# Kernel optimization log

Hardware: AMD Instinct MI355X
Metric: run time of the kernel (lower is better)

The kernel has to match this reference:

```python
import jax, jax.numpy as jnp
import numpy as np

BATCH, SEQ_LEN, D_MODEL = 8, 2048, 1024


def setup_inputs() -> dict:
    key = jax.random.key(0)
    ks = jax.random.split(key, 12)
    s = 0.02  # small init scale (stand-in for xavier)
    D, L = D_MODEL, SEQ_LEN
    return {
        "x": jax.random.normal(ks[0], (BATCH, L, D), jnp.float32),
        "W_B": jax.random.normal(ks[1], (D, D), jnp.float32) * s,
        "b_B": jnp.zeros((D,), jnp.float32),
        "W_C": jax.random.normal(ks[2], (D, D), jnp.float32) * s,
        "b_C": jnp.zeros((D,), jnp.float32),
        "W_d": jax.random.normal(ks[3], (D, D), jnp.float32) * s,
        "b_d": jnp.zeros((D,), jnp.float32),
        "delta_p": jax.random.normal(ks[4], (1, L, D), jnp.float32) * s,  # self.delta
        "A": jax.random.normal(ks[5], (L, D), jnp.float32) * s,
        "W_st": jax.random.normal(ks[6], (D, D), jnp.float32) * s,  # SToken fc1 Linear
        "b_st": jnp.zeros((D,), jnp.float32),
        "st_bias": jax.random.normal(ks[7], (1, 1, D), jnp.float32) * s,  # SToken bias
    }


def reference(x, W_B, b_B, W_C, b_C, W_d, b_d, delta_p, A, W_st, b_st, st_bias):
    # x: [B, L, D]
    z = jax.nn.sigmoid(x)
    B0 = x @ W_B.T + b_B          # LN_B(x)
    C = x @ W_C.T + b_C           # LN_C(x)

    # SToken: squeeze over seq, Linear -> ReLU -> Sigmoid, + bias, * x
    sq = jnp.mean(x, axis=1, keepdims=True)                    # [B, 1, D]
    sq = jax.nn.sigmoid(jax.nn.relu(sq @ W_st.T + b_st))
    T = (sq + st_bias) * x                                     # [B, L, D]

    delta = jax.nn.sigmoid(x @ W_d.T + b_d + delta_p)          # [B, L, D]
    A_ = delta * A                                             # broadcast [L, D]
    B_ = delta * B0

    # diagonal state-space recurrence: s_t = A_t * s_{t-1} + B_t * x_t; y_t = C_t * s_t + T_t
    def step(s, inputs):
        a_t, b_t, c_t, x_t, t_t = inputs                       # each [B, D]
        s = a_t * s + b_t * x_t
        y = c_t * s + t_t
        return s, y

    s0 = jnp.zeros((x.shape[0], x.shape[2]), x.dtype)
    xs = tuple(jnp.swapaxes(a, 0, 1) for a in (A_, B_, C, x, T))  # [L, B, D]
    _, ys = jax.lax.scan(step, s0, xs)
    x_out = jnp.swapaxes(ys, 0, 1) * z                         # [B, L, D]
    return x_out
```

## Files before the change

kernel.cpp:

```cpp
#include <hip/hip_runtime.h>
#include <hip/hip_bf16.h>
#include <cstdint>
#include <cstddef>

#define D_MODEL 1024
#define SEQ     2048
#define BATCH   8
#define M_TOT   (BATCH*SEQ)
#define N_TOT   (3*D_MODEL)
#define K_TOT   D_MODEL
#define KTILES  (K_TOT/64)
#define NCH     64
#define LCH     (SEQ/NCH)
#define W_UP    8

typedef unsigned short u16;
typedef __attribute__((ext_vector_type(8))) short short8;
typedef __attribute__((ext_vector_type(4))) float f32x4;

__device__ __forceinline__ u16 f2bf(float f) {
    __hip_bfloat16 h = __float2bfloat16(f);
    return __builtin_bit_cast(u16, h);
}
__device__ __forceinline__ uint packbf(float lo, float hi) {
    return (uint)f2bf(lo) | ((uint)f2bf(hi) << 16);
}
__device__ __forceinline__ float bf2f(u16 u) {
    __hip_bfloat16 h = __builtin_bit_cast(__hip_bfloat16, u);
    return __bfloat162float(h);
}
__device__ __forceinline__ float sigmoidf(float v) {
    return 1.0f / (1.0f + __expf(-v));
}
__device__ __forceinline__ void gld_lds16(const void* g, void* l) {
    __builtin_amdgcn_global_load_lds((const __attribute__((address_space(1))) void*)g,
                                     (__attribute__((address_space(3))) void*)l, 16, 0, 0);
}
__device__ __forceinline__ void wg_barrier() {
    asm volatile("" ::: "memory");
    __builtin_amdgcn_s_barrier();
    asm volatile("" ::: "memory");
}

__global__ void k_convert(const float* __restrict__ x, u16* __restrict__ xb,
                          float* __restrict__ sq,
                          const float* __restrict__ WB, const float* __restrict__ WC,
                          const float* __restrict__ Wd, u16* __restrict__ wcat,
                          const float* __restrict__ dp, const float* __restrict__ Aar,
                          uint2* __restrict__ dpA) {
    int bid = blockIdx.x;
    if (bid < 512) {
        int tblk = bid & 63, b = bid >> 6;
        int d = threadIdx.x * 4;
        size_t base = ((size_t)b * SEQ + (size_t)tblk * 32) * D_MODEL + d;
        float s0 = 0.f, s1 = 0.f, s2 = 0.f, s3 = 0.f;
        for (int t = 0; t < 32; ++t) {
            float4 v = *(const float4*)&x[base + (size_t)t * D_MODEL];
            s0 += v.x; s1 += v.y; s2 += v.z; s3 += v.w;
            ushort4 o = make_ushort4(f2bf(v.x), f2bf(v.y), f2bf(v.z), f2bf(v.w));
            *(ushort4*)&xb[base + (size_t)t * D_MODEL] = o;
        }
        atomicAdd(&sq[b * D_MODEL + d + 0], s0);
        atomicAdd(&sq[b * D_MODEL + d + 1], s1);
        atomicAdd(&sq[b * D_MODEL + d + 2], s2);
        atomicAdd(&sq[b * D_MODEL + d + 3], s3);
    } else if (bid < 3584) {
        int tg = (bid - 512) * 256 + threadIdx.x;
        size_t e0 = (size_t)tg * 4;
        int n = (int)(e0 >> 10), k0 = (int)(e0 & 1023);
        const float* W = (n < 1024) ? (WB + (size_t)n * 1024)
                       : (n < 2048) ? (WC + (size_t)(n - 1024) * 1024)
                                    : (Wd + (size_t)(n - 2048) * 1024);
        float4 v = *(const float4*)&W[k0];
        wcat[e0 + 0] = f2bf(v.x);
        wcat[e0 + 1] = f2bf(v.y);
        wcat[e0 + 2] = f2bf(v.z);
        wcat[e0 + 3] = f2bf(v.w);
    } else {
        int tg = (bid - 3584) * 256 + threadIdx.x;
        size_t e0 = (size_t)tg * 8;
        float4 d0 = *(const float4*)&dp[e0];
        float4 d1 = *(const float4*)&dp[e0 + 4];
        float4 a0 = *(const float4*)&Aar[e0];
        float4 a1 = *(const float4*)&Aar[e0 + 4];
        uint2* o = &dpA[e0 >> 1];
        o[0] = make_uint2(packbf(d0.x, d0.y), packbf(a0.x, a0.y));
        o[1] = make_uint2(packbf(d0.z, d0.w), packbf(a0.z, a0.w));
        o[2] = make_uint2(packbf(d1.x, d1.y), packbf(a1.x, a1.y));
        o[3] = make_uint2(packbf(d1.z, d1.w), packbf(a1.z, a1.w));
    }
}

__global__ void k_stoken(const float* __restrict__ sq, const float* __restrict__ Wst,
                         float* __restrict__ stacc) {
    __shared__ float s[BATCH][64];
    int nb = blockIdx.x & 3, ks = blockIdx.x >> 2;
    int k0 = ks * 64;
    for (int i = threadIdx.x; i < BATCH * 64; i += 256)
        s[i >> 6][i & 63] = sq[(i >> 6) * D_MODEL + k0 + (i & 63)] * (1.0f / SEQ);
    __syncthreads();
    int n = nb * 256 + threadIdx.x;
    const float* w = Wst + (size_t)n * D_MODEL + k0;
    float acc[BATCH] = {};
    for (int k = 0; k < 64; k += 4) {
        float4 wv = *(const float4*)&w[k];
#pragma unroll
        for (int b = 0; b < BATCH; ++b)
            acc[b] += s[b][k] * wv.x + s[b][k+1] * wv.y + s[b][k+2] * wv.z + s[b][k+3] * wv.w;
    }
#pragma unroll
    for (int b = 0; b < BATCH; ++b)
        atomicAdd(&stacc[b * D_MODEL + n], acc[b]);
}

__device__ __forceinline__ u16* slab_ptr(u16* ls, int buf, int ab, int kk) {
    return ls + (size_t)((((buf << 1) | ab) << 1) | kk) * 8192;
}

__device__ __forceinline__ short8 ldsfrag(const u16* slab, int R, int g) {
    int off = R * 64 + ((g ^ ((R >> 1) & 3)) << 4);
    return *(const short8*)((const char*)slab + off);
}

__device__ __forceinline__ void stage2(const u16* __restrict__ A, const u16* __restrict__ Bm,
                                       u16* ls, int buf, int kk, int ktile,
                                       int i0, int n0, int w, int l) {
    int srow = l >> 2;
    int scol = ((l & 3) ^ ((l >> 3) & 3)) << 4;
    int kbyte = (ktile * 64 + kk * 32) * 2;
    u16* la = slab_ptr(ls, buf, 0, kk);
    u16* lb = slab_ptr(ls, buf, 1, kk);
#pragma unroll
    for (int j = 0; j < 2; ++j) {
        int s = 2 * w + j;
        int row = s * 16 + srow;
        gld_lds16((const char*)(A  + (size_t)(i0 + row) * K_TOT) + kbyte + scol,
                  (char*)la + s * 1024);
        gld_lds16((const char*)(Bm + (size_t)(n0 + row) * K_TOT) + kbyte + scol,
                  (char*)lb + s * 1024);
    }
}

template<bool SG>
__device__ __forceinline__ void kgroup(const u16* __restrict__ A, const u16* __restrict__ Bm,
                                       u16* ls, int t, int i0, int n0,
                                       int wM, int wN, int w, int l, int r, int g,
                                       f32x4 acc[8][4]) {
    const int buf = t & 1;
    const int RA = wM * 128 + r;
    const int RB = wN * 64 + r;

    asm volatile("s_waitcnt vmcnt(0)" ::: "memory");
    wg_barrier();
    if (SG) {
        stage2(A, Bm, ls, buf ^ 1, 0, t + 1, i0, n0, w, l);
        stage2(A, Bm, ls, buf ^ 1, 1, t + 1, i0, n0, w, l);
    }

    const u16* As0 = slab_ptr(ls, buf, 0, 0);
    const u16* Bs0 = slab_ptr(ls, buf, 1, 0);
    const u16* As1 = slab_ptr(ls, buf, 0, 1);
    const u16* Bs1 = slab_ptr(ls, buf, 1, 1);
    short8 a0[4], a1[4], b0[4], b1[4];

#pragma unroll
    for (int m = 0; m < 4; ++m) a0[m] = ldsfrag(As0, RA + m * 16, g);
#pragma unroll
    for (int n = 0; n < 4; ++n) b0[n] = ldsfrag(Bs0, RB + n * 16, g);
#pragma unroll
    for (int m = 0; m < 4; ++m) a1[m] = ldsfrag(As1, RA + m * 16, g);
#pragma unroll
    for (int n = 0; n < 4; ++n) b1[n] = ldsfrag(Bs1, RB + n * 16, g);

    __builtin_amdgcn_s_setprio(1);
#pragma unroll
    for (int m = 0; m < 4; ++m)
#pragma unroll
        for (int n = 0; n < 4; ++n)
            acc[m][n] = __builtin_amdgcn_mfma_f32_16x16x32_bf16(a0[m], b0[n], acc[m][n], 0, 0, 0);
    __builtin_amdgcn_s_setprio(0);

#pragma unroll
    for (int m = 0; m < 4; ++m) a0[m] = ldsfrag(As0, RA + 64 + m * 16, g);

    __builtin_amdgcn_s_setprio(1);
#pragma unroll
    for (int m = 0; m < 4; ++m)
#pragma unroll
        for (int n = 0; n < 4; ++n)
            acc[m][n] = __builtin_amdgcn_mfma_f32_16x16x32_bf16(a1[m], b1[n], acc[m][n], 0, 0, 0);
    __builtin_amdgcn_s_setprio(0);

#pragma unroll
    for (int m = 0; m < 4; ++m) a1[m] = ldsfrag(As1, RA + 64 + m * 16, g);

    __builtin_amdgcn_s_setprio(1);
#pragma unroll
    for (int m = 0; m < 4; ++m)
#pragma unroll
        for (int n = 0; n < 4; ++n)
            acc[4 + m][n] = __builtin_amdgcn_mfma_f32_16x16x32_bf16(a0[m], b0[n], acc[4 + m][n], 0, 0, 0);
#pragma unroll
    for (int m = 0; m < 4; ++m)
#pragma unroll
        for (int n = 0; n < 4; ++n)
            acc[4 + m][n] = __builtin_amdgcn_mfma_f32_16x16x32_bf16(a1[m], b1[n], acc[4 + m][n], 0, 0, 0);
    __builtin_amdgcn_s_setprio(0);
}

__global__ __launch_bounds__(512, 2) void k_gemm(const u16* __restrict__ A,
                                                 const u16* __restrict__ Bm,
                                                 u16* __restrict__ Cout) {
    __shared__ u16 ls[8 * 8192];
    const int tid = threadIdx.x;
    const int l = tid & 63, w = tid >> 6;
    const int wM = w >> 2, wN = w & 3;
    const int r = l & 15, g = l >> 4;
    const int i0 = blockIdx.y * 256;
    const int n0 = blockIdx.x * 256;

    f32x4 acc[8][4] = {};

    stage2(A, Bm, ls, 0, 0, 0, i0, n0, w, l);
    stage2(A, Bm, ls, 0, 1, 0, i0, n0, w, l);

    for (int t = 0; t < KTILES - 1; ++t)
        kgroup<true>(A, Bm, ls, t, i0, n0, wM, wN, w, l, r, g, acc);
    kgroup<false>(A, Bm, ls, KTILES - 1, i0, n0, wM, wN, w, l, r, g, acc);

#pragma unroll
    for (int mi = 0; mi < 8; ++mi)
#pragma unroll
        for (int n = 0; n < 4; ++n)
#pragma unroll
            for (int j = 0; j < 4; ++j) {
                size_t row = (size_t)(i0 + wM * 128 + mi * 16 + g * 4 + j);
                size_t col = (size_t)(n0 + wN * 64 + n * 16 + r);
                Cout[row * N_TOT + col] = f2bf(acc[mi][n][j]);
            }
}

__global__ void k_scan(const u16* __restrict__ xb, const u16* __restrict__ g3,
                       const uint2* __restrict__ dpA,
                       const float* __restrict__ bB, const float* __restrict__ bC,
                       const float* __restrict__ bd, const float* __restrict__ stacc,
                       const float* __restrict__ bst, const float* __restrict__ stb,
                       float* __restrict__ out) {
    int bid = blockIdx.x;
    int dblk = bid & 1, c = (bid >> 1) & (NCH - 1), b = bid >> 7;
    int d = dblk * 512 + threadIdx.x * 2;

    float2 bBv = *(const float2*)&bB[d];
    float2 bdv = *(const float2*)&bd[d];
    float2 bCv = *(const float2*)&bC[d];
    float2 sav = *(const float2*)&stacc[b * D_MODEL + d];
    float2 bstv = *(const float2*)&bst[d];
    float2 stbv = *(const float2*)&stb[d];
    float tc0 = sigmoidf(fmaxf(sav.x + bstv.x, 0.f)) + stbv.x;
    float tc1 = sigmoidf(fmaxf(sav.y + bstv.y, 0.f)) + stbv.y;

    int t0 = c * LCH;
    int tw = (c == 0) ? 0 : t0 - W_UP;
    float s0 = 0.f, s1 = 0.f;

    size_t xoff = ((size_t)b * SEQ + tw) * D_MODEL + d;
    size_t goff = ((size_t)b * SEQ + tw) * N_TOT + d;
    size_t ipa  = ((size_t)tw * D_MODEL + d) >> 1;

    for (int t = tw; t < t0; ++t) {
        uint xu = *(const uint*)&xb[xoff];
        uint gB = *(const uint*)&g3[goff];
        uint gd = *(const uint*)&g3[goff + 2048];
        uint2 pa = dpA[ipa];
        float x0 = bf2f((u16)(xu & 0xffff)), x1 = bf2f((u16)(xu >> 16));
        float b00 = bf2f((u16)(gB & 0xffff)) + bBv.x;
        float b01 = bf2f((u16)(gB >> 16)) + bBv.y;
        float de0 = sigmoidf(bf2f((u16)(gd & 0xffff)) + bdv.x + bf2f((u16)(pa.x & 0xffff)));
        float de1 = sigmoidf(bf2f((u16)(gd >> 16)) + bdv.y + bf2f((u16)(pa.x >> 16)));
        s0 = de0 * bf2f((u16)(pa.y & 0xffff)) * s0 + de0 * b00 * x0;
        s1 = de1 * bf2f((u16)(pa.y >> 16))    * s1 + de1 * b01 * x1;
        xoff += D_MODEL; goff += N_TOT; ipa += D_MODEL / 2;
    }
    for (int t = t0; t < t0 + LCH; ++t) {
        uint xu = *(const uint*)&xb[xoff];
        uint gB = *(const uint*)&g3[goff];
        uint gC = *(const uint*)&g3[goff + 1024];
        uint gd = *(const uint*)&g3[goff + 2048];
        uint2 pa = dpA[ipa];
        float x0 = bf2f((u16)(xu & 0xffff)), x1 = bf2f((u16)(xu >> 16));
        float b00 = bf2f((u16)(gB & 0xffff)) + bBv.x;
        float b01 = bf2f((u16)(gB >> 16)) + bBv.y;
        float de0 = sigmoidf(bf2f((u16)(gd & 0xffff)) + bdv.x + bf2f((u16)(pa.x & 0xffff)));
        float de1 = sigmoidf(bf2f((u16)(gd >> 16)) + bdv.y + bf2f((u16)(pa.x >> 16)));
        s0 = de0 * bf2f((u16)(pa.y & 0xffff)) * s0 + de0 * b00 * x0;
        s1 = de1 * bf2f((u16)(pa.y >> 16))    * s1 + de1 * b01 * x1;
        float c0 = bf2f((u16)(gC & 0xffff)) + bCv.x;
        float c1 = bf2f((u16)(gC >> 16)) + bCv.y;
        float y0 = (c0 * s0 + tc0 * x0) * sigmoidf(x0);
        float y1 = (c1 * s1 + tc1 * x1) * sigmoidf(x1);
        *(float2*)&out[xoff] = make_float2(y0, y1);
        xoff += D_MODEL; goff += N_TOT; ipa += D_MODEL / 2;
    }
}

extern "C" void kernel_launch(void* const* d_in, const int* in_sizes, int n_in,
                              void* d_out, int out_size, void* d_ws, size_t ws_size,
                              hipStream_t stream) {
    const float* x    = (const float*)d_in[0];
    const float* W_B  = (const float*)d_in[1];
    const float* b_B  = (const float*)d_in[2];
    const float* W_C  = (const float*)d_in[3];
    const float* b_C  = (const float*)d_in[4];
    const float* W_d  = (const float*)d_in[5];
    const float* b_d  = (const float*)d_in[6];
    const float* dp   = (const float*)d_in[7];
    const float* Aar  = (const float*)d_in[8];
    const float* W_st = (const float*)d_in[9];
    const float* b_st = (const float*)d_in[10];
    const float* stb  = (const float*)d_in[11];
    float* out = (float*)d_out;

    char* ws = (char*)d_ws;
    u16* xb    = (u16*)ws;   ws += (size_t)M_TOT * K_TOT * 2;
    u16* wcat  = (u16*)ws;   ws += (size_t)N_TOT * K_TOT * 2;
    u16* g3    = (u16*)ws;   ws += (size_t)M_TOT * N_TOT * 2;
    uint2* dpA = (uint2*)ws; ws += (size_t)SEQ * D_MODEL / 2 * 8;
    float* sq    = (float*)ws; ws += (size_t)BATCH * D_MODEL * 4;
    float* stacc = (float*)ws; ws += (size_t)BATCH * D_MODEL * 4;

    hipMemsetAsync(sq, 0, (size_t)2 * BATCH * D_MODEL * 4, stream);
    k_convert<<<4608, 256, 0, stream>>>(x, xb, sq, W_B, W_C, W_d, wcat, dp, Aar, dpA);
    k_stoken<<<64, 256, 0, stream>>>(sq, W_st, stacc);
    k_gemm<<<dim3(N_TOT / 256, M_TOT / 256), 512, 0, stream>>>(xb, wcat, g3);
    k_scan<<<1024, 256, 0, stream>>>(xb, g3, dpA, b_B, b_C, b_d,
                                     stacc, b_st, stb, out);
}
```

Before: 192.0 us.

## Restructure GEMM mainloop into four half-tile stages with finer-grained prefetch waits

Splits each 256x256 block tile into A/B low and high 128-row halves stored in separate LDS regions with a new 128-byte-row swizzle. Each of the four MFMA quadrant phases issues the next k-tile load for one half and waits only on older loads (vmcnt(4)), so global-to-LDS traffic overlaps compute more evenly instead of one full wait per k-tile. Wave-to-output mapping changes so each wave owns strided 64x32 sub-blocks across the quadrants. It adds several extra workgroup barriers per k-tile, which could offset the overlap gain.

```diff
diff --git a/kernel.cpp b/kernel.cpp
--- a/kernel.cpp
+++ b/kernel.cpp
@@ -113,99 +113,125 @@
         atomicAdd(&stacc[b * D_MODEL + n], acc[b]);
 }
 
-__device__ __forceinline__ u16* slab_ptr(u16* ls, int buf, int ab, int kk) {
-    return ls + (size_t)((((buf << 1) | ab) << 1) | kk) * 8192;
-}
-
-__device__ __forceinline__ short8 ldsfrag(const u16* slab, int R, int g) {
-    int off = R * 64 + ((g ^ ((R >> 1) & 3)) << 4);
-    return *(const short8*)((const char*)slab + off);
-}
-
-__device__ __forceinline__ void stage2(const u16* __restrict__ A, const u16* __restrict__ Bm,
-                                       u16* ls, int buf, int kk, int ktile,
-                                       int i0, int n0, int w, int l) {
-    int srow = l >> 2;
-    int scol = ((l & 3) ^ ((l >> 3) & 3)) << 4;
-    int kbyte = (ktile * 64 + kk * 32) * 2;
-    u16* la = slab_ptr(ls, buf, 0, kk);
-    u16* lb = slab_ptr(ls, buf, 1, kk);
+#define HT_AL 0
+#define HT_AH 1
+#define HT_BL 2
+#define HT_BH 3
+
+__device__ __forceinline__ u16* ht_ptr(u16* ls, int buf, int which) {
+    return ls + (size_t)(buf * 4 + which) * 8192;
+}
+
+__device__ __forceinline__ short8 ldsfrag2(const u16* ht, int R, int slot) {
+    int off = R * 128 + ((slot ^ (R & 7)) << 4);
+    return *(const short8*)((const char*)ht + off);
+}
+
+__device__ __forceinline__ void stage_half(const u16* __restrict__ S, u16* dst,
+                                           int rowbase, int ktile, int w, int l) {
+    int rsub = l >> 3;
+    int scol = ((l & 7) ^ rsub) << 4;
+    size_t kbyte = (size_t)ktile * 128;
 #pragma unroll
     for (int j = 0; j < 2; ++j) {
         int s = 2 * w + j;
-        int row = s * 16 + srow;
-        gld_lds16((const char*)(A  + (size_t)(i0 + row) * K_TOT) + kbyte + scol,
-                  (char*)la + s * 1024);
-        gld_lds16((const char*)(Bm + (size_t)(n0 + row) * K_TOT) + kbyte + scol,
-                  (char*)lb + s * 1024);
-    }
-}
-
-template<bool SG>
-__device__ __forceinline__ void kgroup(const u16* __restrict__ A, const u16* __restrict__ Bm,
-                                       u16* ls, int t, int i0, int n0,
-                                       int wM, int wN, int w, int l, int r, int g,
-                                       f32x4 acc[8][4]) {
-    const int buf = t & 1;
-    const int RA = wM * 128 + r;
-    const int RB = wN * 64 + r;
-
-    asm volatile("s_waitcnt vmcnt(0)" ::: "memory");
-    wg_barrier();
-    if (SG) {
-        stage2(A, Bm, ls, buf ^ 1, 0, t + 1, i0, n0, w, l);
-        stage2(A, Bm, ls, buf ^ 1, 1, t + 1, i0, n0, w, l);
-    }
-
-    const u16* As0 = slab_ptr(ls, buf, 0, 0);
-    const u16* Bs0 = slab_ptr(ls, buf, 1, 0);
-    const u16* As1 = slab_ptr(ls, buf, 0, 1);
-    const u16* Bs1 = slab_ptr(ls, buf, 1, 1);
-    short8 a0[4], a1[4], b0[4], b1[4];
-
-#pragma unroll
-    for (int m = 0; m < 4; ++m) a0[m] = ldsfrag(As0, RA + m * 16, g);
-#pragma unroll
-    for (int n = 0; n < 4; ++n) b0[n] = ldsfrag(Bs0, RB + n * 16, g);
-#pragma unroll
-    for (int m = 0; m < 4; ++m) a1[m] = ldsfrag(As1, RA + m * 16, g);
-#pragma unroll
-    for (int n = 0; n < 4; ++n) b1[n] = ldsfrag(Bs1, RB + n * 16, g);
-
+        int row = rowbase + s * 8 + rsub;
+        gld_lds16((const char*)(S + (size_t)row * K_TOT) + kbyte + scol,
+                  (char*)dst + s * 1024);
+    }
+}
+
+template<bool SG, bool LAST>
+__device__ __forceinline__ void kgroup4(const u16* __restrict__ A, const u16* __restrict__ Bm,
+                                        u16* ls, int t, int i0, int n0,
+                                        int wM, int wN, int r, int g, int w, int l,
+                                        f32x4 acc[8][4]) {
+    const int p = t & 1;
+    u16* AL = ht_ptr(ls, p, HT_AL);
+    u16* AH = ht_ptr(ls, p, HT_AH);
+    u16* BL = ht_ptr(ls, p, HT_BL);
+    u16* BH = ht_ptr(ls, p, HT_BH);
+    u16* nAL = ht_ptr(ls, p ^ 1, HT_AL);
+    u16* nAH = ht_ptr(ls, p ^ 1, HT_AH);
+    u16* nBL = ht_ptr(ls, p ^ 1, HT_BL);
+    u16* nBH = ht_ptr(ls, p ^ 1, HT_BH);
+    const int RA = wM * 64 + r;
+    const int RB = wN * 32 + r;
+
+    short8 a[4][2], bl[2][2], bh[2][2];
+
+#pragma unroll
+    for (int m = 0; m < 4; ++m) {
+        a[m][0] = ldsfrag2(AL, RA + m * 16, g);
+        a[m][1] = ldsfrag2(AL, RA + m * 16, 4 + g);
+    }
+#pragma unroll
+    for (int n = 0; n < 2; ++n) {
+        bl[n][0] = ldsfrag2(BL, RB + n * 16, g);
+        bl[n][1] = ldsfrag2(BL, RB + n * 16, 4 + g);
+    }
+    if (SG) stage_half(A, nAL, i0, t + 1, w, l);
+    if (LAST) asm volatile("s_waitcnt vmcnt(0)" ::: "memory");
+    else      asm volatile("s_waitcnt vmcnt(4)" ::: "memory");
+    wg_barrier();
     __builtin_amdgcn_s_setprio(1);
 #pragma unroll
     for (int m = 0; m < 4; ++m)
 #pragma unroll
-        for (int n = 0; n < 4; ++n)
-            acc[m][n] = __builtin_amdgcn_mfma_f32_16x16x32_bf16(a0[m], b0[n], acc[m][n], 0, 0, 0);
+        for (int n = 0; n < 2; ++n)
+            acc[m][n] = __builtin_amdgcn_mfma_f32_16x16x32_bf16(a[m][1], bl[n][1],
+                        __builtin_amdgcn_mfma_f32_16x16x32_bf16(a[m][0], bl[n][0], acc[m][n], 0, 0, 0), 0, 0, 0);
     __builtin_amdgcn_s_setprio(0);
-
-#pragma unroll
-    for (int m = 0; m < 4; ++m) a0[m] = ldsfrag(As0, RA + 64 + m * 16, g);
-
+    wg_barrier();
+
+#pragma unroll
+    for (int n = 0; n < 2; ++n) {
+        bh[n][0] = ldsfrag2(BH, RB + n * 16, g);
+        bh[n][1] = ldsfrag2(BH, RB + n * 16, 4 + g);
+    }
+    if (SG) stage_half(Bm, nBL, n0, t + 1, w, l);
+    if (!LAST) asm volatile("s_waitcnt vmcnt(4)" ::: "memory");
+    wg_barrier();
     __builtin_amdgcn_s_setprio(1);
 #pragma unroll
     for (int m = 0; m < 4; ++m)
 #pragma unroll
-        for (int n = 0; n < 4; ++n)
-            acc[m][n] = __builtin_amdgcn_mfma_f32_16x16x32_bf16(a1[m], b1[n], acc[m][n], 0, 0, 0);
+        for (int n = 0; n < 2; ++n)
+            acc[m][2 + n] = __builtin_amdgcn_mfma_f32_16x16x32_bf16(a[m][1], bh[n][1],
+                            __builtin_amdgcn_mfma_f32_16x16x32_bf16(a[m][0], bh[n][0], acc[m][2 + n], 0, 0, 0), 0, 0, 0);
     __builtin_amdgcn_s_setprio(0);
-
-#pragma unroll
-    for (int m = 0; m < 4; ++m) a1[m] = ldsfrag(As1, RA + 64 + m * 16, g);
-
+    wg_barrier();
+
+#pragma unroll
+    for (int m = 0; m < 4; ++m) {
+        a[m][0] = ldsfrag2(AH, RA + m * 16, g);
+        a[m][1] = ldsfrag2(AH, RA + m * 16, 4 + g);
+    }
+    if (SG) stage_half(Bm, nBH, n0 + 128, t + 1, w, l);
+    if (!LAST) asm volatile("s_waitcnt vmcnt(4)" ::: "memory");
+    wg_barrier();
     __builtin_amdgcn_s_setprio(1);
 #pragma unroll
     for (int m = 0; m < 4; ++m)
 #pragma unroll
-        for (int n = 0; n < 4; ++n)
-            acc[4 + m][n] = __builtin_amdgcn_mfma_f32_16x16x32_bf16(a0[m], b0[n], acc[4 + m][n], 0, 0, 0);
+        for (int n = 0; n < 2; ++n)
+            acc[4 + m][n] = __builtin_amdgcn_mfma_f32_16x16x32_bf16(a[m][1], bl[n][1],
+                            __builtin_amdgcn_mfma_f32_16x16x32_bf16(a[m][0], bl[n][0], acc[4 + m][n], 0, 0, 0), 0, 0, 0);
+    __builtin_amdgcn_s_setprio(0);
+    wg_barrier();
+
+    if (SG) stage_half(A, nAH, i0 + 128, t + 1, w, l);
+    if (!LAST) asm volatile("s_waitcnt vmcnt(4)" ::: "memory");
+    wg_barrier();
+    __builtin_amdgcn_s_setprio(1);
 #pragma unroll
     for (int m = 0; m < 4; ++m)
 #pragma unroll
-        for (int n = 0; n < 4; ++n)
-            acc[4 + m][n] = __builtin_amdgcn_mfma_f32_16x16x32_bf16(a1[m], b1[n], acc[4 + m][n], 0, 0, 0);
+        for (int n = 0; n < 2; ++n)
+            acc[4 + m][2 + n] = __builtin_amdgcn_mfma_f32_16x16x32_bf16(a[m][1], bh[n][1],
+                                __builtin_amdgcn_mfma_f32_16x16x32_bf16(a[m][0], bh[n][0], acc[4 + m][2 + n], 0, 0, 0), 0, 0, 0);
     __builtin_amdgcn_s_setprio(0);
+    wg_barrier();
 }
 
 __global__ __launch_bounds__(512, 2) void k_gemm(const u16* __restrict__ A,
@@ -221,22 +247,26 @@
 
     f32x4 acc[8][4] = {};
 
-    stage2(A, Bm, ls, 0, 0, 0, i0, n0, w, l);
-    stage2(A, Bm, ls, 0, 1, 0, i0, n0, w, l);
+    stage_half(A,  ht_ptr(ls, 0, HT_AL), i0,       0, w, l);
+    stage_half(Bm, ht_ptr(ls, 0, HT_BL), n0,       0, w, l);
+    stage_half(Bm, ht_ptr(ls, 0, HT_BH), n0 + 128, 0, w, l);
+    stage_half(A,  ht_ptr(ls, 0, HT_AH), i0 + 128, 0, w, l);
+    asm volatile("s_waitcnt vmcnt(4)" ::: "memory");
+    wg_barrier();
 
     for (int t = 0; t < KTILES - 1; ++t)
-        kgroup<true>(A, Bm, ls, t, i0, n0, wM, wN, w, l, r, g, acc);
-    kgroup<false>(A, Bm, ls, KTILES - 1, i0, n0, wM, wN, w, l, r, g, acc);
+        kgroup4<true, false>(A, Bm, ls, t, i0, n0, wM, wN, r, g, w, l, acc);
+    kgroup4<false, true>(A, Bm, ls, KTILES - 1, i0, n0, wM, wN, r, g, w, l, acc);
 
 #pragma unroll
     for (int mi = 0; mi < 8; ++mi)
 #pragma unroll
-        for (int n = 0; n < 4; ++n)
+        for (int nj = 0; nj < 4; ++nj)
 #pragma unroll
             for (int j = 0; j < 4; ++j) {
-                size_t row = (size_t)(i0 + wM * 128 + mi * 16 + g * 4 + j);
-                size_t col = (size_t)(n0 + wN * 64 + n * 16 + r);
-                Cout[row * N_TOT + col] = f2bf(acc[mi][n][j]);
+                size_t row = (size_t)(i0 + (mi >> 2) * 128 + wM * 64 + (mi & 3) * 16 + g * 4 + j);
+                size_t col = (size_t)(n0 + (nj >> 1) * 128 + wN * 32 + (nj & 1) * 16 + r);
+                Cout[row * N_TOT + col] = f2bf(acc[mi][nj][j]);
             }
 }
 
```

Result: no change. 190.3 us (-0.9%).
